# Kernel tuning notes

Hardware: AMD Instinct MI355X
Metric: run time of the kernel (lower is better)

Reference implementation:

```python
import jax, jax.numpy as jnp
import numpy as np

N = 50000
IN_FEATS = 128
H_FEATS = 256
E = 800000


def setup_inputs() -> dict:
    key = jax.random.key(0)
    ks = jax.random.split(key, 8)
    x = jax.random.normal(ks[0], (N, IN_FEATS), dtype=jnp.float32)
    edge_index = jax.random.randint(ks[1], (2, E), 0, N, dtype=jnp.int64)
    s1 = 1.0 / np.sqrt(IN_FEATS)
    s2 = 1.0 / np.sqrt(H_FEATS)
    # PyG SAGEConv: lin_l (applied to aggregated neighbors, with bias), lin_r (root, no bias)
    W1_l = jax.random.uniform(ks[2], (H_FEATS, IN_FEATS), jnp.float32, -s1, s1)
    b1_l = jax.random.uniform(ks[3], (H_FEATS,), jnp.float32, -s1, s1)
    W1_r = jax.random.uniform(ks[4], (H_FEATS, IN_FEATS), jnp.float32, -s1, s1)
    W2_l = jax.random.uniform(ks[5], (1, H_FEATS), jnp.float32, -s2, s2)
    b2_l = jax.random.uniform(ks[6], (1,), jnp.float32, -s2, s2)
    W2_r = jax.random.uniform(ks[7], (1, H_FEATS), jnp.float32, -s2, s2)
    return {"x": x, "edge_index": edge_index, "W1_l": W1_l, "b1_l": b1_l,
            "W1_r": W1_r, "W2_l": W2_l, "b2_l": b2_l, "W2_r": W2_r}


def _mean_aggregate(feat, src, dst, n_nodes):
    # scatter-mean of source features onto destination nodes
    summed = jax.ops.segment_sum(feat[src], dst, num_segments=n_nodes)
    deg = jax.ops.segment_sum(jnp.ones((src.shape[0],), feat.dtype), dst,
                              num_segments=n_nodes)
    return summed / jnp.maximum(deg, 1.0)[:, None]


def reference(x, edge_index, W1_l, b1_l, W1_r, W2_l, b2_l, W2_r):
    src, dst = edge_index[0], edge_index[1]
    n = x.shape[0]
    # SAGEConv 1: lin_l(mean_agg(x)) + lin_r(x), then ReLU (dropout is identity at eval)
    agg1 = _mean_aggregate(x, src, dst, n)
    h = jax.nn.relu(agg1 @ W1_l.T + b1_l + x @ W1_r.T)
    # SAGEConv 2 -> scalar per node
    agg2 = _mean_aggregate(h, src, dst, n)
    out = (agg2 @ W2_l.T + b2_l + h @ W2_r.T).reshape(-1)
    return out
```

## Files before the change

kernel.cpp:

```cpp
#include <hip/hip_runtime.h>

static constexpr int IN_F   = 128;
static constexpr int ECH    = 4096;
static constexpr int RSLOT  = 64;
static constexpr int CAPB   = 5376;
static constexpr int CSR_CAP = 5376;
static constexpr int OVF_CAP = 4096;

typedef __attribute__((ext_vector_type(8))) short bf16x8;
typedef __attribute__((ext_vector_type(8))) unsigned short u16x8;
typedef __attribute__((ext_vector_type(4))) float f32x4;

__device__ inline unsigned short f2bf(float f) {
    unsigned u = __float_as_uint(f);
    u += 0x7FFF + ((u >> 16) & 1);
    return (unsigned short)(u >> 16);
}
__device__ inline float bf2f(unsigned short h) {
    return __uint_as_float(((unsigned)h) << 16);
}

__global__ __launch_bounds__(256) void edge_bin(const int* __restrict__ src,
        const int* __restrict__ dst, unsigned* __restrict__ btmp,
        int* __restrict__ rcnt, int* __restrict__ ovf_cnt, unsigned* __restrict__ ovf,
        int E) {
    __shared__ unsigned stage[ECH];
    __shared__ int h[256], lcur[256];
    int tid = threadIdx.x, eb = blockIdx.x;
    int base = eb * ECH;
    h[tid] = 0; lcur[tid] = 0;
    __syncthreads();
#pragma unroll
    for (int r = 0; r < ECH / 256; r++) {
        int e = base + r * 256 + tid;
        if (e < E) {
            unsigned d = (unsigned)dst[e];
            stage[r * 256 + tid] = (d << 16) | (unsigned)src[e];
            atomicAdd(&h[d >> 8], 1);
        }
    }
    __syncthreads();
    int hv = h[tid];
    rcnt[eb * 256 + tid] = hv < RSLOT ? hv : RSLOT;
#pragma unroll
    for (int r = 0; r < ECH / 256; r++) {
        int e = base + r * 256 + tid;
        if (e < E) {
            unsigned pk = stage[r * 256 + tid];
            int bkt = pk >> 24;
            int rank = atomicAdd(&lcur[bkt], 1);
            if (rank < RSLOT)
                btmp[(size_t)(eb * 256 + bkt) * RSLOT + rank] = pk;
            else {
                int pos = atomicAdd(ovf_cnt, 1);
                if (pos < OVF_CAP) ovf[pos] = pk;
            }
        }
    }
}

__global__ __launch_bounds__(256) void bucket_csr(const unsigned* __restrict__ btmp,
        const int* __restrict__ rcnt, const int* __restrict__ ovf_cnt,
        const unsigned* __restrict__ ovf,
        int* __restrict__ rowbeg, int* __restrict__ degn, int* __restrict__ col,
        int n, int nblk) {
    __shared__ unsigned stage[CSR_CAP];
    __shared__ unsigned colL[CSR_CAP];
    __shared__ int cntL[256], curL[256];
    __shared__ int ws[4];
    __shared__ int s_extra;
    int b = blockIdx.x, tid = threadIdx.x, lane = tid & 63, wid = tid >> 6;

    int rc = (tid < nblk) ? rcnt[tid * 256 + b] : 0;
    int val = rc;
#pragma unroll
    for (int off = 1; off < 64; off <<= 1) {
        int t = __shfl_up(val, off);
        if (lane >= off) val += t;
    }
    if (lane == 63) ws[wid] = val;
    if (tid == 0) s_extra = 0;
    cntL[tid] = 0;
    __syncthreads();
    int pre = 0;
    for (int w = 0; w < wid; w++) pre += ws[w];
    int rb  = pre + val - rc;
    int cnt = ws[0] + ws[1] + ws[2] + ws[3];
    if (tid < nblk && rc > 0) {
        const unsigned* sp = btmp + (size_t)(tid * 256 + b) * RSLOT;
        for (int i = 0; i < rc; i++) stage[rb + i] = sp[i];
    }
    __syncthreads();
    int novf = *ovf_cnt;
    if (novf > 0) {
        if (novf > OVF_CAP) novf = OVF_CAP;
        for (int i = tid; i < novf; i += 256) {
            unsigned pk = ovf[i];
            if ((int)(pk >> 24) == b) {
                int pos = atomicAdd(&s_extra, 1);
                if (cnt + pos < CSR_CAP) stage[cnt + pos] = pk;
            }
        }
    }
    __syncthreads();
    cnt += s_extra;
    if (cnt > CSR_CAP) cnt = CSR_CAP;
    for (int i = tid; i < cnt; i += 256) atomicAdd(&cntL[(stage[i] >> 16) & 255], 1);
    __syncthreads();
    int v = cntL[tid];
    int val2 = v;
#pragma unroll
    for (int off = 1; off < 64; off <<= 1) {
        int t = __shfl_up(val2, off);
        if (lane >= off) val2 += t;
    }
    if (lane == 63) ws[wid] = val2;
    __syncthreads();
    pre = 0;
    for (int w = 0; w < wid; w++) pre += ws[w];
    int ex = pre + val2 - v;
    curL[tid] = ex;
    int node = b * 256 + tid;
    if (node < n) { rowbeg[node] = b * CAPB + ex; degn[node] = v; }
    __syncthreads();
    for (int i = tid; i < cnt; i += 256) {
        unsigned pk = stage[i];
        int pos = atomicAdd(&curL[(pk >> 16) & 255], 1);
        colL[pos] = pk & 0xFFFFu;
    }
    __syncthreads();
    for (int i = tid; i < cnt; i += 256) col[b * CAPB + i] = (int)colL[i];
}

__global__ __launch_bounds__(256) void split_xw(const float* __restrict__ x,
        const float* __restrict__ W1l, const float* __restrict__ W1r,
        unsigned short* __restrict__ xh,
        unsigned short* __restrict__ Wh, unsigned short* __restrict__ Wl,
        long long total2) {
    long long i = (long long)blockIdx.x * 256 + threadIdx.x;
    if (i < total2) {
        float2 v = ((const float2*)x)[i];
        ((ushort2*)xh)[i] = make_ushort2(f2bf(v.x), f2bf(v.y));
    } else {
        long long wi = i - total2;
        if (wi < 65536) {
            int feat = (int)(wi >> 8), k = (int)(wi & 255);
            float w = (k < IN_F) ? W1l[feat * IN_F + k] : W1r[feat * IN_F + (k - IN_F)];
            unsigned short h = f2bf(w);
            Wh[wi] = h;
            Wl[wi] = f2bf(w - bf2f(h));
        }
    }
}

__global__ void agg1_kernel(const unsigned short* __restrict__ xh,
                            const int* __restrict__ rowbeg, const int* __restrict__ degn,
                            const int* __restrict__ col,
                            unsigned short* __restrict__ aggh, int n) {
    int gid  = blockIdx.x * blockDim.x + threadIdx.x;
    int node = gid >> 5;
    int l32  = threadIdx.x & 31;
    if (node >= n) return;
    int beg = rowbeg[node], dg = degn[node], end = beg + dg;
    float a0 = 0.f, a1 = 0.f, a2 = 0.f, a3 = 0.f;
    int j = beg;
    for (; j + 3 < end; j += 4) {
        int4 cs = *(const int4*)(col + j);
        ushort4 v0 = ((const ushort4*)(xh + (size_t)cs.x * IN_F))[l32];
        ushort4 v1 = ((const ushort4*)(xh + (size_t)cs.y * IN_F))[l32];
        ushort4 v2 = ((const ushort4*)(xh + (size_t)cs.z * IN_F))[l32];
        ushort4 v3 = ((const ushort4*)(xh + (size_t)cs.w * IN_F))[l32];
        a0 += bf2f(v0.x) + bf2f(v1.x) + bf2f(v2.x) + bf2f(v3.x);
        a1 += bf2f(v0.y) + bf2f(v1.y) + bf2f(v2.y) + bf2f(v3.y);
        a2 += bf2f(v0.z) + bf2f(v1.z) + bf2f(v2.z) + bf2f(v3.z);
        a3 += bf2f(v0.w) + bf2f(v1.w) + bf2f(v2.w) + bf2f(v3.w);
    }
    for (; j < end; j++) {
        ushort4 v0 = ((const ushort4*)(xh + (size_t)col[j] * IN_F))[l32];
        a0 += bf2f(v0.x); a1 += bf2f(v0.y); a2 += bf2f(v0.z); a3 += bf2f(v0.w);
    }
    float inv = 1.0f / fmaxf((float)dg, 1.0f);
    ushort4 hi;
    hi.x = f2bf(a0 * inv); hi.y = f2bf(a1 * inv);
    hi.z = f2bf(a2 * inv); hi.w = f2bf(a3 * inv);
    ((ushort4*)(aggh + (size_t)node * IN_F))[l32] = hi;
}

__global__ __launch_bounds__(256, 2) void layer1_kernel(
        const unsigned short* __restrict__ xh,
        const unsigned short* __restrict__ aggh,
        const unsigned short* __restrict__ Wh, const unsigned short* __restrict__ Wl,
        const float* __restrict__ b1l,
        const float* __restrict__ W2l, const float* __restrict__ W2r,
        float* __restrict__ p, float* __restrict__ q, int n) {
    __shared__ unsigned short Ah[128 * 32];
    __shared__ unsigned short Bh[256 * 32];
    __shared__ unsigned short Bl[256 * 32];

    int tid  = threadIdx.x;
    int lane = tid & 63;
    int wv   = tid >> 6;
    int m15  = lane & 15;
    int quad = lane >> 4;
    int node0 = blockIdx.x * 128;

    f32x4 acc[2][16];
#pragma unroll
    for (int nt = 0; nt < 2; nt++)
#pragma unroll
        for (int ft = 0; ft < 16; ft++) acc[nt][ft] = (f32x4){0.f, 0.f, 0.f, 0.f};

    int rown = tid >> 2;
    int sub  = tid & 3;

    for (int kc = 0; kc < 8; kc++) {
        int k0 = kc * 32;
        const unsigned short* Ahs = (kc < 4) ? aggh : xh;
        int aoff = (kc < 4) ? k0 : (k0 - IN_F);

#pragma unroll
        for (int ps = 0; ps < 2; ps++) {
            int nl = ps * 64 + rown;
            int g  = node0 + nl;
            u16x8 hv = {0,0,0,0,0,0,0,0};
            if (g < n) hv = *(const u16x8*)(Ahs + (size_t)g * IN_F + aoff + sub * 8);
            *(u16x8*)&Ah[nl * 32 + sub * 8] = hv;
        }
#pragma unroll
        for (int ps = 0; ps < 4; ps++) {
            int feat = ps * 64 + rown;
            size_t go = (size_t)feat * 256 + k0 + sub * 8;
            *(u16x8*)&Bh[feat * 32 + sub * 8] = *(const u16x8*)(Wh + go);
            *(u16x8*)&Bl[feat * 32 + sub * 8] = *(const u16x8*)(Wl + go);
        }
        __syncthreads();

        bf16x8 a0h = *(const bf16x8*)&Ah[(wv * 32 + m15) * 32 + quad * 8];
        bf16x8 a1h = *(const bf16x8*)&Ah[(wv * 32 + 16 + m15) * 32 + quad * 8];
#pragma unroll
        for (int ft = 0; ft < 16; ft++) {
            bf16x8 bh = *(const bf16x8*)&Bh[(ft * 16 + m15) * 32 + quad * 8];
            bf16x8 bl = *(const bf16x8*)&Bl[(ft * 16 + m15) * 32 + quad * 8];
            acc[0][ft] = __builtin_amdgcn_mfma_f32_16x16x32_bf16(a0h, bh, acc[0][ft], 0, 0, 0);
            acc[0][ft] = __builtin_amdgcn_mfma_f32_16x16x32_bf16(a0h, bl, acc[0][ft], 0, 0, 0);
            acc[1][ft] = __builtin_amdgcn_mfma_f32_16x16x32_bf16(a1h, bh, acc[1][ft], 0, 0, 0);
            acc[1][ft] = __builtin_amdgcn_mfma_f32_16x16x32_bf16(a1h, bl, acc[1][ft], 0, 0, 0);
        }
        __syncthreads();
    }

#pragma unroll
    for (int nt = 0; nt < 2; nt++) {
        float u0 = 0, u1 = 0, u2 = 0, u3 = 0;
        float v0 = 0, v1 = 0, v2 = 0, v3 = 0;
#pragma unroll
        for (int ft = 0; ft < 16; ft++) {
            int fj = ft * 16 + m15;
            float bb = b1l[fj], wl = W2l[fj], wr = W2r[fj];
            f32x4 c = acc[nt][ft];
            float h0 = fmaxf(c[0] + bb, 0.f);
            float h1 = fmaxf(c[1] + bb, 0.f);
            float h2 = fmaxf(c[2] + bb, 0.f);
            float h3 = fmaxf(c[3] + bb, 0.f);
            u0 += h0 * wl; v0 += h0 * wr;
            u1 += h1 * wl; v1 += h1 * wr;
            u2 += h2 * wl; v2 += h2 * wr;
            u3 += h3 * wl; v3 += h3 * wr;
        }
#pragma unroll
        for (int off = 1; off < 16; off <<= 1) {
            u0 += __shfl_xor(u0, off); v0 += __shfl_xor(v0, off);
            u1 += __shfl_xor(u1, off); v1 += __shfl_xor(v1, off);
            u2 += __shfl_xor(u2, off); v2 += __shfl_xor(v2, off);
            u3 += __shfl_xor(u3, off); v3 += __shfl_xor(v3, off);
        }
        if (m15 == 0) {
            int nb = node0 + wv * 32 + nt * 16 + quad * 4;
            if (nb + 0 < n) { p[nb + 0] = u0; q[nb + 0] = v0; }
            if (nb + 1 < n) { p[nb + 1] = u1; q[nb + 1] = v1; }
            if (nb + 2 < n) { p[nb + 2] = u2; q[nb + 2] = v2; }
            if (nb + 3 < n) { p[nb + 3] = u3; q[nb + 3] = v3; }
        }
    }
}

__global__ void out_kernel(const float* __restrict__ p, const float* __restrict__ q,
                           const int* __restrict__ rowbeg, const int* __restrict__ degn,
                           const int* __restrict__ col,
                           const float* __restrict__ b2l,
                           float* __restrict__ out, int n) {
    int gid  = blockIdx.x * blockDim.x + threadIdx.x;
    int node = gid >> 4;
    int l    = threadIdx.x & 15;
    if (node >= n) return;
    int beg = rowbeg[node], dg = degn[node], end = beg + dg;
    float s = 0.f;
    for (int j = beg + l; j < end; j += 16) s += p[col[j]];
#pragma unroll
    for (int off = 8; off; off >>= 1) s += __shfl_xor(s, off);
    if (l == 0) {
        float inv = 1.0f / fmaxf((float)dg, 1.0f);
        out[node] = s * inv + b2l[0] + q[node];
    }
}

extern "C" void kernel_launch(void* const* d_in, const int* in_sizes, int n_in,
                              void* d_out, int out_size, void* d_ws, size_t ws_size,
                              hipStream_t stream) {
    const float* x   = (const float*)d_in[0];
    const int*   ei  = (const int*)  d_in[1];
    const float* W1l = (const float*)d_in[2];
    const float* b1l = (const float*)d_in[3];
    const float* W1r = (const float*)d_in[4];
    const float* W2l = (const float*)d_in[5];
    const float* b2l = (const float*)d_in[6];
    const float* W2r = (const float*)d_in[7];
    float* out = (float*)d_out;

    int n = in_sizes[0] / IN_F;
    int E = in_sizes[1] / 2;
    const int* src = ei;
    const int* dst = ei + E;

    size_t n_pad = ((size_t)n + 256) & ~(size_t)255;
    int nbk  = (n + 255) >> 8;
    int nblk = (E + ECH - 1) / ECH;

    int* ovf_cnt   = (int*)d_ws;
    unsigned* ovf  = (unsigned*)(ovf_cnt + 64);
    int* rcnt      = (int*)(ovf + OVF_CAP);
    int* rowbeg    = rcnt + 65536;
    int* degn      = rowbeg + n_pad;
    unsigned* btmp = (unsigned*)(degn + n_pad);
    int* col       = (int*)(btmp + (size_t)nblk * 256 * RSLOT);
    unsigned short* Whs = (unsigned short*)(col + (size_t)nbk * CAPB + 192);
    unsigned short* Wls  = Whs + 65536;
    unsigned short* xh   = Wls + 65536;
    unsigned short* aggh = xh + (size_t)n * IN_F;
    float* p = (float*)(aggh + (size_t)n * IN_F);
    float* q = p + n_pad;

    hipMemsetAsync(ovf_cnt, 0, sizeof(int), stream);

    edge_bin<<<nblk, 256, 0, stream>>>(src, dst, btmp, rcnt, ovf_cnt, ovf, E);
    bucket_csr<<<nbk, 256, 0, stream>>>(btmp, rcnt, ovf_cnt, ovf,
                                        rowbeg, degn, col, n, nblk);

    long long total2 = (long long)n * IN_F / 2;
    long long tot = total2 + 65536;
    split_xw<<<(int)((tot + 255) / 256), 256, 0, stream>>>(
        x, W1l, W1r, xh, Whs, Wls, total2);

    agg1_kernel<<<(int)(((size_t)n * 32 + 255) / 256), 256, 0, stream>>>(
        xh, rowbeg, degn, col, aggh, n);

    layer1_kernel<<<(n + 127) / 128, 256, 0, stream>>>(
        xh, aggh, Whs, Wls, b1l, W2l, W2r, p, q, n);

    out_kernel<<<(int)(((size_t)n * 16 + 255) / 256), 256, 0, stream>>>(
        p, q, rowbeg, degn, col, b2l, out, n);
}
```

Baseline: 167.1 us.

## Fuse edge binning with bf16 conversion, widen agg1 loads, drop A LDS staging

Merges the edge-binning kernel and the x/W bf16 split kernel into one launch whose blocks branch on block index, removing a launch and letting the two independent jobs run concurrently. The first-layer aggregation now uses 16 lanes per node with 16-byte loads instead of 32 lanes with 8-byte loads. The layer-1 GEMM loads A fragments straight from global memory into registers rather than staging them through shared memory, and its occupancy hint is raised from 2 to 4 blocks. Trade-offs include different register pressure under the new launch bound and less gather parallelism per node.

```diff
diff --git a/kernel.cpp b/kernel.cpp
--- a/kernel.cpp
+++ b/kernel.cpp
@@ -20,40 +20,63 @@
     return __uint_as_float(((unsigned)h) << 16);
 }
 
-__global__ __launch_bounds__(256) void edge_bin(const int* __restrict__ src,
+__global__ __launch_bounds__(256) void prep_kernel(const int* __restrict__ src,
         const int* __restrict__ dst, unsigned* __restrict__ btmp,
         int* __restrict__ rcnt, int* __restrict__ ovf_cnt, unsigned* __restrict__ ovf,
-        int E) {
+        int E, int nblk,
+        const float* __restrict__ x,
+        const float* __restrict__ W1l, const float* __restrict__ W1r,
+        unsigned short* __restrict__ xh,
+        unsigned short* __restrict__ Wh, unsigned short* __restrict__ Wl,
+        long long total2) {
     __shared__ unsigned stage[ECH];
     __shared__ int h[256], lcur[256];
-    int tid = threadIdx.x, eb = blockIdx.x;
-    int base = eb * ECH;
-    h[tid] = 0; lcur[tid] = 0;
-    __syncthreads();
-#pragma unroll
-    for (int r = 0; r < ECH / 256; r++) {
-        int e = base + r * 256 + tid;
-        if (e < E) {
-            unsigned d = (unsigned)dst[e];
-            stage[r * 256 + tid] = (d << 16) | (unsigned)src[e];
-            atomicAdd(&h[d >> 8], 1);
-        }
-    }
-    __syncthreads();
-    int hv = h[tid];
-    rcnt[eb * 256 + tid] = hv < RSLOT ? hv : RSLOT;
-#pragma unroll
-    for (int r = 0; r < ECH / 256; r++) {
-        int e = base + r * 256 + tid;
-        if (e < E) {
-            unsigned pk = stage[r * 256 + tid];
-            int bkt = pk >> 24;
-            int rank = atomicAdd(&lcur[bkt], 1);
-            if (rank < RSLOT)
-                btmp[(size_t)(eb * 256 + bkt) * RSLOT + rank] = pk;
-            else {
-                int pos = atomicAdd(ovf_cnt, 1);
-                if (pos < OVF_CAP) ovf[pos] = pk;
+    int tid = threadIdx.x;
+    if ((int)blockIdx.x < nblk) {
+        int eb = blockIdx.x;
+        int base = eb * ECH;
+        h[tid] = 0; lcur[tid] = 0;
+        __syncthreads();
+#pragma unroll
+        for (int r = 0; r < ECH / 256; r++) {
+            int e = base + r * 256 + tid;
+            if (e < E) {
+                unsigned d = (unsigned)dst[e];
+                stage[r * 256 + tid] = (d << 16) | (unsigned)src[e];
+                atomicAdd(&h[d >> 8], 1);
+            }
+        }
+        __syncthreads();
+        int hv = h[tid];
+        rcnt[eb * 256 + tid] = hv < RSLOT ? hv : RSLOT;
+#pragma unroll
+        for (int r = 0; r < ECH / 256; r++) {
+            int e = base + r * 256 + tid;
+            if (e < E) {
+                unsigned pk = stage[r * 256 + tid];
+                int bkt = pk >> 24;
+                int rank = atomicAdd(&lcur[bkt], 1);
+                if (rank < RSLOT)
+                    btmp[(size_t)(eb * 256 + bkt) * RSLOT + rank] = pk;
+                else {
+                    int pos = atomicAdd(ovf_cnt, 1);
+                    if (pos < OVF_CAP) ovf[pos] = pk;
+                }
+            }
+        }
+    } else {
+        long long i = (long long)(blockIdx.x - nblk) * 256 + tid;
+        if (i < total2) {
+            float2 v = ((const float2*)x)[i];
+            ((ushort2*)xh)[i] = make_ushort2(f2bf(v.x), f2bf(v.y));
+        } else {
+            long long wi = i - total2;
+            if (wi < 65536) {
+                int feat = (int)(wi >> 8), k = (int)(wi & 255);
+                float w = (k < IN_F) ? W1l[feat * IN_F + k] : W1r[feat * IN_F + (k - IN_F)];
+                unsigned short hh = f2bf(w);
+                Wh[wi] = hh;
+                Wl[wi] = f2bf(w - bf2f(hh));
             }
         }
     }
@@ -132,68 +155,54 @@
     for (int i = tid; i < cnt; i += 256) col[b * CAPB + i] = (int)colL[i];
 }
 
-__global__ __launch_bounds__(256) void split_xw(const float* __restrict__ x,
-        const float* __restrict__ W1l, const float* __restrict__ W1r,
-        unsigned short* __restrict__ xh,
-        unsigned short* __restrict__ Wh, unsigned short* __restrict__ Wl,
-        long long total2) {
-    long long i = (long long)blockIdx.x * 256 + threadIdx.x;
-    if (i < total2) {
-        float2 v = ((const float2*)x)[i];
-        ((ushort2*)xh)[i] = make_ushort2(f2bf(v.x), f2bf(v.y));
-    } else {
-        long long wi = i - total2;
-        if (wi < 65536) {
-            int feat = (int)(wi >> 8), k = (int)(wi & 255);
-            float w = (k < IN_F) ? W1l[feat * IN_F + k] : W1r[feat * IN_F + (k - IN_F)];
-            unsigned short h = f2bf(w);
-            Wh[wi] = h;
-            Wl[wi] = f2bf(w - bf2f(h));
-        }
-    }
-}
-
 __global__ void agg1_kernel(const unsigned short* __restrict__ xh,
                             const int* __restrict__ rowbeg, const int* __restrict__ degn,
                             const int* __restrict__ col,
                             unsigned short* __restrict__ aggh, int n) {
     int gid  = blockIdx.x * blockDim.x + threadIdx.x;
-    int node = gid >> 5;
-    int l32  = threadIdx.x & 31;
+    int node = gid >> 4;
+    int l16  = threadIdx.x & 15;
     if (node >= n) return;
     int beg = rowbeg[node], dg = degn[node], end = beg + dg;
     float a0 = 0.f, a1 = 0.f, a2 = 0.f, a3 = 0.f;
+    float a4 = 0.f, a5 = 0.f, a6 = 0.f, a7 = 0.f;
     int j = beg;
     for (; j + 3 < end; j += 4) {
         int4 cs = *(const int4*)(col + j);
-        ushort4 v0 = ((const ushort4*)(xh + (size_t)cs.x * IN_F))[l32];
-        ushort4 v1 = ((const ushort4*)(xh + (size_t)cs.y * IN_F))[l32];
-        ushort4 v2 = ((const ushort4*)(xh + (size_t)cs.z * IN_F))[l32];
-        ushort4 v3 = ((const ushort4*)(xh + (size_t)cs.w * IN_F))[l32];
-        a0 += bf2f(v0.x) + bf2f(v1.x) + bf2f(v2.x) + bf2f(v3.x);
-        a1 += bf2f(v0.y) + bf2f(v1.y) + bf2f(v2.y) + bf2f(v3.y);
-        a2 += bf2f(v0.z) + bf2f(v1.z) + bf2f(v2.z) + bf2f(v3.z);
-        a3 += bf2f(v0.w) + bf2f(v1.w) + bf2f(v2.w) + bf2f(v3.w);
+        u16x8 v0 = ((const u16x8*)(xh + (size_t)cs.x * IN_F))[l16];
+        u16x8 v1 = ((const u16x8*)(xh + (size_t)cs.y * IN_F))[l16];
+        u16x8 v2 = ((const u16x8*)(xh + (size_t)cs.z * IN_F))[l16];
+        u16x8 v3 = ((const u16x8*)(xh + (size_t)cs.w * IN_F))[l16];
+        a0 += bf2f(v0[0]) + bf2f(v1[0]) + bf2f(v2[0]) + bf2f(v3[0]);
+        a1 += bf2f(v0[1]) + bf2f(v1[1]) + bf2f(v2[1]) + bf2f(v3[1]);
+        a2 += bf2f(v0[2]) + bf2f(v1[2]) + bf2f(v2[2]) + bf2f(v3[2]);
+        a3 += bf2f(v0[3]) + bf2f(v1[3]) + bf2f(v2[3]) + bf2f(v3[3]);
+        a4 += bf2f(v0[4]) + bf2f(v1[4]) + bf2f(v2[4]) + bf2f(v3[4]);
+        a5 += bf2f(v0[5]) + bf2f(v1[5]) + bf2f(v2[5]) + bf2f(v3[5]);
+        a6 += bf2f(v0[6]) + bf2f(v1[6]) + bf2f(v2[6]) + bf2f(v3[6]);
+        a7 += bf2f(v0[7]) + bf2f(v1[7]) + bf2f(v2[7]) + bf2f(v3[7]);
     }
     for (; j < end; j++) {
-        ushort4 v0 = ((const ushort4*)(xh + (size_t)col[j] * IN_F))[l32];
-        a0 += bf2f(v0.x); a1 += bf2f(v0.y); a2 += bf2f(v0.z); a3 += bf2f(v0.w);
+        u16x8 v0 = ((const u16x8*)(xh + (size_t)col[j] * IN_F))[l16];
+        a0 += bf2f(v0[0]); a1 += bf2f(v0[1]); a2 += bf2f(v0[2]); a3 += bf2f(v0[3]);
+        a4 += bf2f(v0[4]); a5 += bf2f(v0[5]); a6 += bf2f(v0[6]); a7 += bf2f(v0[7]);
     }
     float inv = 1.0f / fmaxf((float)dg, 1.0f);
-    ushort4 hi;
-    hi.x = f2bf(a0 * inv); hi.y = f2bf(a1 * inv);
-    hi.z = f2bf(a2 * inv); hi.w = f2bf(a3 * inv);
-    ((ushort4*)(aggh + (size_t)node * IN_F))[l32] = hi;
-}
-
-__global__ __launch_bounds__(256, 2) void layer1_kernel(
+    u16x8 hi;
+    hi[0] = f2bf(a0 * inv); hi[1] = f2bf(a1 * inv);
+    hi[2] = f2bf(a2 * inv); hi[3] = f2bf(a3 * inv);
+    hi[4] = f2bf(a4 * inv); hi[5] = f2bf(a5 * inv);
+    hi[6] = f2bf(a6 * inv); hi[7] = f2bf(a7 * inv);
+    ((u16x8*)(aggh + (size_t)node * IN_F))[l16] = hi;
+}
+
+__global__ __launch_bounds__(256, 4) void layer1_kernel(
         const unsigned short* __restrict__ xh,
         const unsigned short* __restrict__ aggh,
         const unsigned short* __restrict__ Wh, const unsigned short* __restrict__ Wl,
         const float* __restrict__ b1l,
         const float* __restrict__ W2l, const float* __restrict__ W2r,
         float* __restrict__ p, float* __restrict__ q, int n) {
-    __shared__ unsigned short Ah[128 * 32];
     __shared__ unsigned short Bh[256 * 32];
     __shared__ unsigned short Bl[256 * 32];
 
@@ -213,19 +222,19 @@
     int rown = tid >> 2;
     int sub  = tid & 3;
 
+    int g0 = node0 + wv * 32 + m15;
+    int g1 = g0 + 16;
+
     for (int kc = 0; kc < 8; kc++) {
         int k0 = kc * 32;
-        const unsigned short* Ahs = (kc < 4) ? aggh : xh;
+        const unsigned short* Asrc = (kc < 4) ? aggh : xh;
         int aoff = (kc < 4) ? k0 : (k0 - IN_F);
 
-#pragma unroll
-        for (int ps = 0; ps < 2; ps++) {
-            int nl = ps * 64 + rown;
-            int g  = node0 + nl;
-            u16x8 hv = {0,0,0,0,0,0,0,0};
-            if (g < n) hv = *(const u16x8*)(Ahs + (size_t)g * IN_F + aoff + sub * 8);
-            *(u16x8*)&Ah[nl * 32 + sub * 8] = hv;
-        }
+        u16x8 za = {0,0,0,0,0,0,0,0};
+        u16x8 a0u = za, a1u = za;
+        if (g0 < n) a0u = *(const u16x8*)(Asrc + (size_t)g0 * IN_F + aoff + quad * 8);
+        if (g1 < n) a1u = *(const u16x8*)(Asrc + (size_t)g1 * IN_F + aoff + quad * 8);
+
 #pragma unroll
         for (int ps = 0; ps < 4; ps++) {
             int feat = ps * 64 + rown;
@@ -235,8 +244,8 @@
         }
         __syncthreads();
 
-        bf16x8 a0h = *(const bf16x8*)&Ah[(wv * 32 + m15) * 32 + quad * 8];
-        bf16x8 a1h = *(const bf16x8*)&Ah[(wv * 32 + 16 + m15) * 32 + quad * 8];
+        bf16x8 a0h = (bf16x8)a0u;
+        bf16x8 a1h = (bf16x8)a1u;
 #pragma unroll
         for (int ft = 0; ft < 16; ft++) {
             bf16x8 bh = *(const bf16x8*)&Bh[(ft * 16 + m15) * 32 + quad * 8];
@@ -342,16 +351,16 @@
 
     hipMemsetAsync(ovf_cnt, 0, sizeof(int), stream);
 
-    edge_bin<<<nblk, 256, 0, stream>>>(src, dst, btmp, rcnt, ovf_cnt, ovf, E);
+    long long total2 = (long long)n * IN_F / 2;
+    int split_blocks = (int)((total2 + 65536 + 255) / 256);
+    prep_kernel<<<nblk + split_blocks, 256, 0, stream>>>(
+        src, dst, btmp, rcnt, ovf_cnt, ovf, E, nblk,
+        x, W1l, W1r, xh, Whs, Wls, total2);
+
     bucket_csr<<<nbk, 256, 0, stream>>>(btmp, rcnt, ovf_cnt, ovf,
                                         rowbeg, degn, col, n, nblk);
 
-    long long total2 = (long long)n * IN_F / 2;
-    long long tot = total2 + 65536;
-    split_xw<<<(int)((tot + 255) / 256), 256, 0, stream>>>(
-        x, W1l, W1r, xh, Whs, Wls, total2);
-
-    agg1_kernel<<<(int)(((size_t)n * 32 + 255) / 256), 256, 0, stream>>>(
+    agg1_kernel<<<(int)(((size_t)n * 16 + 255) / 256), 256, 0, stream>>>(
         xh, rowbeg, degn, col, aggh, n);
 
     layer1_kernel<<<(n + 127) / 128, 256, 0, stream>>>(
```

Measured after the change: 212.5 us. +27.1%, slower.
